# Performance work log

Hardware: AMD Instinct MI355X
Metric: run time of the kernel (lower is better)

Reference implementation:

```python
import jax, jax.numpy as jnp
import numpy as np

NUM_NODES = 100000
NODE_CH = 3     # node_fiber_channels (degree-0)
EDGE_CH = 3     # edge_fiber_channels (degree-0)
MID = 32        # RadialProfile hidden dim (NVIDIA SE3-Transformer default)
VALUE_CH = 1    # fiber_out channels // channels_div = 3 // 2
KQ_CH = 1       # key/query channels (match value fiber on shared degrees)
BATCH = 64


def setup_inputs() -> dict:
    key = jax.random.key(0)
    ks = jax.random.split(key, 8)
    s = 0.1
    return {
        "input_data": jax.random.normal(ks[0], (BATCH, 3, NUM_NODES, 3), jnp.float32),
        # RadialProfile MLP: edge_feats -> MID -> MID -> (VALUE_CH+KQ_CH)*NODE_CH (last layer no bias)
        "W1": jax.random.normal(ks[1], (EDGE_CH, MID), jnp.float32) * s,
        "b1": jnp.zeros((MID,), jnp.float32),
        "W2": jax.random.normal(ks[2], (MID, MID), jnp.float32) * s,
        "b2": jnp.zeros((MID,), jnp.float32),
        "W3": jax.random.normal(ks[3], (MID, (VALUE_CH + KQ_CH) * NODE_CH), jnp.float32) * s,
        # LinearSE3 query (deg 0): (KQ_CH, NODE_CH)
        "Wq": jax.random.normal(ks[4], (KQ_CH, NODE_CH), jnp.float32) * s,
        # LinearSE3 project after cat-skip: (NODE_CH, VALUE_CH + NODE_CH)
        "Wp": jax.random.normal(ks[5], (NODE_CH, VALUE_CH + NODE_CH), jnp.float32) * s,
    }


def reference(input_data, W1, b1, W2, b2, W3, Wq, Wp):
    B, C, N, _ = input_data.shape
    node = input_data[:, 0]               # (B, N, 3) degree-0 node feats
    edge = input_data[:, 2]               # (B, E=N, 3) degree-0 edge feats
    src = jnp.arange(N)                   # ring graph: i -> (i+1) % N
    dst = (src + 1) % N

    # ConvSE3 deg0->deg0 (to_key_value): radial MLP on invariant edge feats
    # produces a per-edge (out_ch, in_ch) matrix applied to source-node feats.
    h = jax.nn.relu(edge @ W1 + b1)
    h = jax.nn.relu(h @ W2 + b2)
    R = (h @ W3).reshape(B, N, VALUE_CH + KQ_CH, NODE_CH)      # (B,E,2,3)
    kv = jnp.einsum('beoc,bec->beo', R, node[:, src])          # (B,E,2)
    value = kv[..., 0]                                         # chunk: value first
    key_e = kv[..., 1]                                         # key second

    # LinearSE3 query at nodes
    q = jnp.einsum('bnc,kc->bnk', node, Wq)[..., 0]            # (B,N)

    # AttentionSE3: dot(key, query[dst]) / sqrt(key feats), softmax over
    # incoming edges of each destination node (ring: exactly one per node).
    logits = key_e * q[:, dst] / jnp.sqrt(jnp.float32(KQ_CH))  # (B,E)
    m = jnp.full((B, N), -jnp.inf, logits.dtype).at[:, dst].max(logits)
    ex = jnp.exp(logits - m[:, dst])
    denom = jnp.zeros((B, N), logits.dtype).at[:, dst].add(ex)
    alpha = ex / denom[:, dst]
    z = jnp.zeros((B, N), logits.dtype).at[:, dst].add(alpha * value)  # (B,N)

    # aggregate_residual 'cat' ([attn_out, node]) then LinearSE3 project
    feat = jnp.concatenate([z[..., None], node], axis=-1)      # (B,N,4)
    out0 = jnp.einsum('bnc,oc->bno', feat, Wp)                 # (B,N,3)

    # channels 1 and 2 pass through unchanged
    return input_data.at[:, 0].set(out0)
```

## Files before the change

kernel.cpp:

```cpp
#include <hip/hip_runtime.h>

#define N_NODES 100000
#define BATCH   64
#define MID     32
#define LSTRIDE 80
#define TOTAL   (BATCH * N_NODES)

typedef __attribute__((ext_vector_type(2))) __fp16 h2v;
typedef _Float16 __attribute__((ext_vector_type(8))) f16x8;
typedef float __attribute__((ext_vector_type(4))) f32x4;
typedef float __attribute__((ext_vector_type(2))) f32x2;

union H2U  { h2v h; unsigned int u; };
union U4H8 { uint4 u; f16x8 h; };

struct __attribute__((packed, aligned(4))) F4u { f32x4 v; };
struct __attribute__((packed, aligned(4))) F2u { f32x2 v; };

__host__ __device__ __forceinline__ int jperm(int k) { return (k & 1) ? 16 + (k >> 1) : (k >> 1); }

__global__ void prep_weights(const float* __restrict__ W1, const float* __restrict__ b1,
                             const float* __restrict__ W2, const float* __restrict__ W3,
                             uint4* __restrict__ wf, unsigned int* __restrict__ aux) {
    int t = threadIdx.x;
    if (t < 128) {
        int grp = t >> 6, l = t & 63;
        int j = (l & 15) + 16 * grp, k0 = (l >> 4) * 8;
        unsigned int pk[4];
#pragma unroll
        for (int m = 0; m < 4; ++m) {
            H2U a; a.h = __builtin_amdgcn_cvt_pkrtz(W2[(k0 + 2*m) * MID + j],
                                                    W2[(k0 + 2*m + 1) * MID + j]);
            pk[m] = a.u;
        }
        wf[t] = make_uint4(pk[0], pk[1], pk[2], pk[3]);
    } else if (t < 192) {
        int l = t & 63;
        int j = l & 15, k0 = (l >> 4) * 8;
        unsigned int pk[4];
#pragma unroll
        for (int m = 0; m < 4; ++m) {
            int ja = jperm(k0 + 2*m), jb = jperm(k0 + 2*m + 1);
            float x0 = (j < 3) ? W3[ja * 6 + j] : 0.f;
            float x1 = (j < 3) ? W3[jb * 6 + j] : 0.f;
            H2U a; a.h = __builtin_amdgcn_cvt_pkrtz(x0, x1);
            pk[m] = a.u;
        }
        wf[128 + l] = make_uint4(pk[0], pk[1], pk[2], pk[3]);
    } else if (t < 240) {
        int i = t - 192;
        int k = i >> 4, m = i & 15;
        H2U a; a.h = __builtin_amdgcn_cvt_pkrtz(W1[k * MID + 2*m], W1[k * MID + 2*m + 1]);
        aux[i] = a.u;
    } else {
        int m = t - 240;
        H2U a; a.h = __builtin_amdgcn_cvt_pkrtz(b1[2*m], b1[2*m + 1]);
        aux[48 + m] = a.u;
    }
}

__global__ __launch_bounds__(256) void xattn_kernel(
    const float* __restrict__ in,
    const unsigned int* __restrict__ aux,
    const float* __restrict__ b2,
    const uint4* __restrict__ wf,
    const float* __restrict__ Wp,
    float* __restrict__ out)
{
    __shared__ uint4 ldsbuf[4 * 64 * LSTRIDE / 16];
    int tid  = threadIdx.x;
    int lane = tid & 63;
    int wave = tid >> 6;
    char* L = (char*)ldsbuf + wave * (64 * LSTRIDE);

    int idx = blockIdx.x * 256 + tid;
    int b = idx / N_NODES;
    int n = idx - b * N_NODES;
    bool last = (idx == TOTAL - 1);

    const float* inb  = in  + (size_t)b * (3u * N_NODES * 3u);
    float*       outb = out + (size_t)b * (3u * N_NODES * 3u);

    f32x4 ndv = ((const F4u*)(inb + (size_t)n * 3))->v;
    f32x4 c1v = ((const F4u*)(inb + (size_t)N_NODES * 3 + (size_t)n * 3))->v;
    f32x4 edv;
    const float* e_ptr = inb + (size_t)2 * N_NODES * 3 + (size_t)n * 3;
    if (!last) {
        edv = ((const F4u*)e_ptr)->v;
    } else {
        edv = (f32x4){e_ptr[0], e_ptr[1], e_ptr[2], 0.f};
    }

    float qn0 = ndv.x, qn1 = ndv.y, qn2 = ndv.z;
    float ed0 = edv.x, ed1 = edv.y, ed2 = edv.z;

    {
        float* o1p = outb + (size_t)N_NODES * 3 + (size_t)n * 3;
        ((F4u*)o1p)->v = c1v;
        float* o2p = outb + (size_t)2 * N_NODES * 3 + (size_t)n * 3;
        if (!last) ((F4u*)o2p)->v = edv;
        else { o2p[0] = ed0; o2p[1] = ed1; o2p[2] = ed2; }
    }

    float pp0 = __shfl_up(qn0, 1), pp1 = __shfl_up(qn1, 1), pp2 = __shfl_up(qn2, 1);
    float e0  = __shfl_up(ed0, 1), e1  = __shfl_up(ed1, 1), e2  = __shfl_up(ed2, 1);
    if (lane == 0 || n == 0) {
        int p = (n == 0) ? (N_NODES - 1) : (n - 1);
        const float* np_ = inb + (size_t)p * 3;
        const float* epp = inb + ((size_t)2 * N_NODES + p) * 3;
        pp0 = np_[0]; pp1 = np_[1]; pp2 = np_[2];
        e0  = epp[0]; e1  = epp[1]; e2  = epp[2];
    }

    h2v eh0 = {(__fp16)e0, (__fp16)e0};
    h2v eh1 = {(__fp16)e1, (__fp16)e1};
    h2v eh2 = {(__fp16)e2, (__fp16)e2};
    h2v zz  = {(__fp16)0.0f, (__fp16)0.0f};
    unsigned int hp[16];
#pragma unroll
    for (int m = 0; m < 16; ++m) {
        H2U acc, w0, w1_, w2_;
        acc.u = aux[48 + m];
        w0.u  = aux[m];
        w1_.u = aux[16 + m];
        w2_.u = aux[32 + m];
        acc.h = eh0 * w0.h + acc.h;
        acc.h = eh1 * w1_.h + acc.h;
        acc.h = eh2 * w2_.h + acc.h;
        acc.h = __builtin_elementwise_max(acc.h, zz);
        hp[m] = acc.u;
    }
    {
        uint4* row = (uint4*)(L + lane * LSTRIDE);
        row[0] = make_uint4(hp[0],  hp[1],  hp[2],  hp[3]);
        row[1] = make_uint4(hp[4],  hp[5],  hp[6],  hp[7]);
        row[2] = make_uint4(hp[8],  hp[9],  hp[10], hp[11]);
        row[3] = make_uint4(hp[12], hp[13], hp[14], hp[15]);
    }

    int r16 = lane & 15;
    int q4  = lane >> 4;
    U4H8 wb20; wb20.u = wf[lane];
    U4H8 wb21; wb21.u = wf[64 + lane];
    U4H8 wb3;  wb3.u  = wf[128 + lane];
    float bias0 = b2[r16], bias1 = b2[16 + r16];

#pragma unroll
    for (int pt = 0; pt < 4; ++pt) {
        U4H8 a; a.u = *(const uint4*)(L + (pt*16 + r16) * LSTRIDE + q4 * 16);
        f32x4 acc0 = {bias0, bias0, bias0, bias0};
        f32x4 acc1 = {bias1, bias1, bias1, bias1};
        acc0 = __builtin_amdgcn_mfma_f32_16x16x32_f16(a.h, wb20.h, acc0, 0, 0, 0);
        acc1 = __builtin_amdgcn_mfma_f32_16x16x32_f16(a.h, wb21.h, acc1, 0, 0, 0);

        unsigned int* tb = (unsigned int*)(L + (pt*16 + q4*4) * LSTRIDE) + r16;
#pragma unroll
        for (int r = 0; r < 4; ++r) {
            H2U t;
            t.h = __builtin_amdgcn_cvt_pkrtz(acc0[r], acc1[r]);
            t.h = __builtin_elementwise_max(t.h, zz);
            tb[r * (LSTRIDE/4)] = t.u;
        }

        U4H8 a3; a3.u = *(const uint4*)(L + (pt*16 + r16) * LSTRIDE + q4 * 16);
        f32x4 c3 = __builtin_amdgcn_mfma_f32_16x16x32_f16(a3.h, wb3.h, (f32x4){0.f,0.f,0.f,0.f}, 0, 0, 0);

        if (r16 < 3)
            *(f32x4*)(L + r16 * 256 + (pt*16 + q4*4) * 4) = c3;
    }

    float r0 = *(const float*)(L + 0*256 + lane*4);
    float r1 = *(const float*)(L + 1*256 + lane*4);
    float r2 = *(const float*)(L + 2*256 + lane*4);
    float z  = fmaf(r0, pp0, fmaf(r1, pp1, r2 * pp2));

    float vo[3];
#pragma unroll
    for (int o = 0; o < 3; ++o) {
        float v = Wp[o*4 + 0] * z;
        v = fmaf(Wp[o*4 + 1], qn0, v);
        v = fmaf(Wp[o*4 + 2], qn1, v);
        v = fmaf(Wp[o*4 + 3], qn2, v);
        vo[o] = v;
    }
    float* o0 = outb + (size_t)n * 3;
    ((F2u*)o0)->v = (f32x2){vo[0], vo[1]};
    o0[2] = vo[2];
}

extern "C" void kernel_launch(void* const* d_in, const int* in_sizes, int n_in,
                              void* d_out, int out_size, void* d_ws, size_t ws_size,
                              hipStream_t stream) {
    const float* in = (const float*)d_in[0];
    const float* W1 = (const float*)d_in[1];
    const float* b1 = (const float*)d_in[2];
    const float* W2 = (const float*)d_in[3];
    const float* b2 = (const float*)d_in[4];
    const float* W3 = (const float*)d_in[5];
    const float* Wp = (const float*)d_in[7];
    float* out = (float*)d_out;

    uint4* wf = (uint4*)d_ws;
    unsigned int* aux = (unsigned int*)(wf + 192);
    hipLaunchKernelGGL(prep_weights, dim3(1), dim3(256), 0, stream, W1, b1, W2, W3, wf, aux);

    int blocks = TOTAL / 256;
    hipLaunchKernelGGL(xattn_kernel, dim3(blocks), dim3(256), 0, stream,
                       in, aux, b2, wf, Wp, out);
}
```

Baseline: 95.37 us.

## Chain MFMA layers in registers via transposed operands and pack shuffles in fp16

Swaps the MFMA operand order so the second layer's output lands in registers already laid out as the B operand of the third layer. This removes the LDS write-back and re-read between the two matmuls. Neighbour node and edge features are packed as fp16 pairs, cutting the lane shuffles from six to three. The bias is loaded as a vector, and the final R values go through a small fp16 LDS buffer. The cost is reduced precision for the neighbour node features and the R outputs, now fp16 instead of fp32.

After: 95.55 us. No clear change (+0.2%).

```diff
diff --git a/kernel.cpp b/kernel.cpp
--- a/kernel.cpp
+++ b/kernel.cpp
@@ -4,6 +4,7 @@
 #define BATCH   64
 #define MID     32
 #define LSTRIDE 80
+#define WLDS    (64 * LSTRIDE + 512)
 #define TOTAL   (BATCH * N_NODES)
 
 typedef __attribute__((ext_vector_type(2))) __fp16 h2v;
@@ -16,8 +17,6 @@
 
 struct __attribute__((packed, aligned(4))) F4u { f32x4 v; };
 struct __attribute__((packed, aligned(4))) F2u { f32x2 v; };
-
-__host__ __device__ __forceinline__ int jperm(int k) { return (k & 1) ? 16 + (k >> 1) : (k >> 1); }
 
 __global__ void prep_weights(const float* __restrict__ W1, const float* __restrict__ b1,
                              const float* __restrict__ W2, const float* __restrict__ W3,
@@ -36,15 +35,15 @@
         wf[t] = make_uint4(pk[0], pk[1], pk[2], pk[3]);
     } else if (t < 192) {
         int l = t & 63;
-        int j = l & 15, k0 = (l >> 4) * 8;
+        int c = l & 15, q4 = l >> 4;
         unsigned int pk[4];
 #pragma unroll
-        for (int m = 0; m < 4; ++m) {
-            int ja = jperm(k0 + 2*m), jb = jperm(k0 + 2*m + 1);
-            float x0 = (j < 3) ? W3[ja * 6 + j] : 0.f;
-            float x1 = (j < 3) ? W3[jb * 6 + j] : 0.f;
+        for (int mp = 0; mp < 4; ++mp) {
+            int jb = (mp < 2) ? (4*q4 + 2*mp) : (16 + 4*q4 + 2*(mp - 2));
+            float x0 = (c < 3) ? W3[jb * 6 + c] : 0.f;
+            float x1 = (c < 3) ? W3[(jb + 1) * 6 + c] : 0.f;
             H2U a; a.h = __builtin_amdgcn_cvt_pkrtz(x0, x1);
-            pk[m] = a.u;
+            pk[mp] = a.u;
         }
         wf[128 + l] = make_uint4(pk[0], pk[1], pk[2], pk[3]);
     } else if (t < 240) {
@@ -67,16 +66,18 @@
     const float* __restrict__ Wp,
     float* __restrict__ out)
 {
-    __shared__ uint4 ldsbuf[4 * 64 * LSTRIDE / 16];
+    __shared__ __attribute__((aligned(16))) char ldsbuf[4 * WLDS];
     int tid  = threadIdx.x;
     int lane = tid & 63;
     int wave = tid >> 6;
-    char* L = (char*)ldsbuf + wave * (64 * LSTRIDE);
+    char* L  = ldsbuf + wave * WLDS;
+    char* ZB = L + 64 * LSTRIDE;
 
     int idx = blockIdx.x * 256 + tid;
     int b = idx / N_NODES;
     int n = idx - b * N_NODES;
     bool last = (idx == TOTAL - 1);
+    bool btail = (n == N_NODES - 1);
 
     const float* inb  = in  + (size_t)b * (3u * N_NODES * 3u);
     float*       outb = out + (size_t)b * (3u * N_NODES * 3u);
@@ -85,37 +86,43 @@
     f32x4 c1v = ((const F4u*)(inb + (size_t)N_NODES * 3 + (size_t)n * 3))->v;
     f32x4 edv;
     const float* e_ptr = inb + (size_t)2 * N_NODES * 3 + (size_t)n * 3;
-    if (!last) {
-        edv = ((const F4u*)e_ptr)->v;
-    } else {
-        edv = (f32x4){e_ptr[0], e_ptr[1], e_ptr[2], 0.f};
-    }
+    if (!last) edv = ((const F4u*)e_ptr)->v;
+    else       edv = (f32x4){e_ptr[0], e_ptr[1], e_ptr[2], 0.f};
 
     float qn0 = ndv.x, qn1 = ndv.y, qn2 = ndv.z;
-    float ed0 = edv.x, ed1 = edv.y, ed2 = edv.z;
 
     {
         float* o1p = outb + (size_t)N_NODES * 3 + (size_t)n * 3;
         ((F4u*)o1p)->v = c1v;
         float* o2p = outb + (size_t)2 * N_NODES * 3 + (size_t)n * 3;
-        if (!last) ((F4u*)o2p)->v = edv;
-        else { o2p[0] = ed0; o2p[1] = ed1; o2p[2] = ed2; }
-    }
-
-    float pp0 = __shfl_up(qn0, 1), pp1 = __shfl_up(qn1, 1), pp2 = __shfl_up(qn2, 1);
-    float e0  = __shfl_up(ed0, 1), e1  = __shfl_up(ed1, 1), e2  = __shfl_up(ed2, 1);
+        if (!btail) ((F4u*)o2p)->v = edv;
+        else { o2p[0] = edv.x; o2p[1] = edv.y; o2p[2] = edv.z; }
+    }
+
+    H2U s0_, s1_, s2_;
+    s0_.h = __builtin_amdgcn_cvt_pkrtz(qn0, qn1);
+    s1_.h = __builtin_amdgcn_cvt_pkrtz(qn2, edv.x);
+    s2_.h = __builtin_amdgcn_cvt_pkrtz(edv.y, edv.z);
+    unsigned int t0 = __shfl_up(s0_.u, 1);
+    unsigned int t1 = __shfl_up(s1_.u, 1);
+    unsigned int t2 = __shfl_up(s2_.u, 1);
     if (lane == 0 || n == 0) {
         int p = (n == 0) ? (N_NODES - 1) : (n - 1);
         const float* np_ = inb + (size_t)p * 3;
         const float* epp = inb + ((size_t)2 * N_NODES + p) * 3;
-        pp0 = np_[0]; pp1 = np_[1]; pp2 = np_[2];
-        e0  = epp[0]; e1  = epp[1]; e2  = epp[2];
-    }
-
-    h2v eh0 = {(__fp16)e0, (__fp16)e0};
-    h2v eh1 = {(__fp16)e1, (__fp16)e1};
-    h2v eh2 = {(__fp16)e2, (__fp16)e2};
-    h2v zz  = {(__fp16)0.0f, (__fp16)0.0f};
+        H2U a, bb, c;
+        a.h  = __builtin_amdgcn_cvt_pkrtz(np_[0], np_[1]);
+        bb.h = __builtin_amdgcn_cvt_pkrtz(np_[2], epp[0]);
+        c.h  = __builtin_amdgcn_cvt_pkrtz(epp[1], epp[2]);
+        t0 = a.u; t1 = bb.u; t2 = c.u;
+    }
+    H2U u0, u1, u2; u0.u = t0; u1.u = t1; u2.u = t2;
+    float pp0 = (float)u0.h[0], pp1 = (float)u0.h[1], pp2 = (float)u1.h[0];
+    h2v eh0 = {u1.h[1], u1.h[1]};
+    h2v eh1 = {u2.h[0], u2.h[0]};
+    h2v eh2 = {u2.h[1], u2.h[1]};
+
+    h2v zz = {(__fp16)0.0f, (__fp16)0.0f};
     unsigned int hp[16];
 #pragma unroll
     for (int m = 0; m < 16; ++m) {
@@ -143,36 +150,38 @@
     U4H8 wb20; wb20.u = wf[lane];
     U4H8 wb21; wb21.u = wf[64 + lane];
     U4H8 wb3;  wb3.u  = wf[128 + lane];
-    float bias0 = b2[r16], bias1 = b2[16 + r16];
+    f32x4 bi0 = *(const f32x4*)(b2 + 4*q4);
+    f32x4 bi1 = *(const f32x4*)(b2 + 16 + 4*q4);
 
 #pragma unroll
     for (int pt = 0; pt < 4; ++pt) {
-        U4H8 a; a.u = *(const uint4*)(L + (pt*16 + r16) * LSTRIDE + q4 * 16);
-        f32x4 acc0 = {bias0, bias0, bias0, bias0};
-        f32x4 acc1 = {bias1, bias1, bias1, bias1};
-        acc0 = __builtin_amdgcn_mfma_f32_16x16x32_f16(a.h, wb20.h, acc0, 0, 0, 0);
-        acc1 = __builtin_amdgcn_mfma_f32_16x16x32_f16(a.h, wb21.h, acc1, 0, 0, 0);
-
-        unsigned int* tb = (unsigned int*)(L + (pt*16 + q4*4) * LSTRIDE) + r16;
-#pragma unroll
-        for (int r = 0; r < 4; ++r) {
-            H2U t;
-            t.h = __builtin_amdgcn_cvt_pkrtz(acc0[r], acc1[r]);
-            t.h = __builtin_elementwise_max(t.h, zz);
-            tb[r * (LSTRIDE/4)] = t.u;
+        U4H8 hB; hB.u = *(const uint4*)(L + (pt*16 + r16) * LSTRIDE + q4 * 16);
+        f32x4 acc0 = bi0;
+        f32x4 acc1 = bi1;
+        acc0 = __builtin_amdgcn_mfma_f32_16x16x32_f16(wb20.h, hB.h, acc0, 0, 0, 0);
+        acc1 = __builtin_amdgcn_mfma_f32_16x16x32_f16(wb21.h, hB.h, acc1, 0, 0, 0);
+
+        H2U g0, g1, g2, g3;
+        g0.h = __builtin_elementwise_max(__builtin_amdgcn_cvt_pkrtz(acc0[0], acc0[1]), zz);
+        g1.h = __builtin_elementwise_max(__builtin_amdgcn_cvt_pkrtz(acc0[2], acc0[3]), zz);
+        g2.h = __builtin_elementwise_max(__builtin_amdgcn_cvt_pkrtz(acc1[0], acc1[1]), zz);
+        g3.h = __builtin_elementwise_max(__builtin_amdgcn_cvt_pkrtz(acc1[2], acc1[3]), zz);
+        U4H8 b3f; b3f.u = make_uint4(g0.u, g1.u, g2.u, g3.u);
+
+        f32x4 c3 = __builtin_amdgcn_mfma_f32_16x16x32_f16(wb3.h, b3f.h,
+                                                          (f32x4){0.f,0.f,0.f,0.f}, 0, 0, 0);
+
+        if (q4 == 0) {
+            H2U za; za.h = __builtin_amdgcn_cvt_pkrtz(c3[0], c3[1]);
+            H2U zb; zb.h = __builtin_amdgcn_cvt_pkrtz(c3[2], 0.f);
+            *(uint2*)(ZB + (pt*16 + r16) * 8) = make_uint2(za.u, zb.u);
         }
-
-        U4H8 a3; a3.u = *(const uint4*)(L + (pt*16 + r16) * LSTRIDE + q4 * 16);
-        f32x4 c3 = __builtin_amdgcn_mfma_f32_16x16x32_f16(a3.h, wb3.h, (f32x4){0.f,0.f,0.f,0.f}, 0, 0, 0);
-
-        if (r16 < 3)
-            *(f32x4*)(L + r16 * 256 + (pt*16 + q4*4) * 4) = c3;
-    }
-
-    float r0 = *(const float*)(L + 0*256 + lane*4);
-    float r1 = *(const float*)(L + 1*256 + lane*4);
-    float r2 = *(const float*)(L + 2*256 + lane*4);
-    float z  = fmaf(r0, pp0, fmaf(r1, pp1, r2 * pp2));
+    }
+
+    uint2 zr = *(const uint2*)(ZB + lane * 8);
+    H2U za, zb; za.u = zr.x; zb.u = zr.y;
+    float z = fmaf((float)za.h[0], pp0,
+              fmaf((float)za.h[1], pp1, (float)zb.h[0] * pp2));
 
     float vo[3];
 #pragma unroll
```
